# Performance work log

Hardware: AMD Instinct MI355X
Metric: run time of the kernel (lower is better)

## Reference

```python
import jax, jax.numpy as jnp
import numpy as np
import jax.scipy.signal as jss

SX, SY, C, K = 256, 256, 3, 10
C0 = [0, 0, 0, 1, 1, 1, 2, 2, 2, 0]
C1 = [[0, 1, 2, 9], [3, 4, 5], [6, 7, 8]]
DD, DT, SIGMA = 5, 0.2, 0.65

_KX = jnp.array([[-1., 0., 1.], [-2., 0., 2.], [-1., 0., 1.]])
_KY = _KX.T


def _conv2(A, Kf):
    # zero-padded 'same' 2D true convolution, vmapped over channel axis
    return jax.vmap(lambda a: jss.convolve2d(a, Kf, mode='same'), in_axes=2, out_axes=2)(A)


def sobel(A):
    # (X, Y, c) -> (X, Y, 2, c): [sobel_y, sobel_x] stacked on axis 2 (FlowLenia convention)
    return jnp.concatenate([_conv2(A, _KY)[:, :, None, :], _conv2(A, _KX)[:, :, None, :]], axis=2)


def growth(U, m, s):
    # bell(U,m,s)*2 - 1
    return jnp.exp(-((U - m) / s) ** 2 / 2.) * 2. - 1.


def get_kernels_fft(R, r, a, w, b):
    # FlowLenia kernel construction: ring distance -> smooth cutoff * sum-of-bumps, normalized, fft2(fftshift)
    mid = SX // 2
    xs = jnp.arange(-mid, mid, dtype=jnp.float32)
    D = jnp.sqrt(xs[:, None] ** 2 + xs[None, :] ** 2)            # (X, Y)
    Dk = D[..., None] / ((R + 15.) * r)                          # (X, Y, k)
    ker = (b * jnp.exp(-(Dk[..., None] - a) ** 2 / w)).sum(-1)   # (X, Y, k)
    sig = 0.5 * (jnp.tanh(-(Dk - 1.) * 10. / 2.) + 1.)           # sigmoid(-(D-1)*10)
    Kk = sig * ker
    nK = Kk / Kk.sum(axis=(0, 1), keepdims=True)
    return jnp.fft.fft2(jnp.fft.fftshift(nK, axes=(0, 1)), axes=(0, 1))


def _rt_apply(A, F):
    # Reintegration tracking with 'wall' border: flow-driven mass redistribution over a (2dd+1)^2 neighborhood
    ii = jnp.arange(SX, dtype=jnp.float32)
    pos = jnp.stack(jnp.meshgrid(ii, ii, indexing='ij'), axis=-1) + 0.5   # (X, Y, 2) cell centers
    ma = DD - SIGMA                                   # max flow magnitude
    mu = pos[..., None] + jnp.clip(DT * F, -ma, ma)   # (X, Y, 2, C) target centers
    mu = jnp.clip(mu, SIGMA, SX - SIGMA)              # wall border
    offs = jnp.arange(-DD, DD + 1)
    gx, gy = jnp.meshgrid(offs, offs, indexing='ij')
    dxs, dys = gx.reshape(-1), gy.reshape(-1)
    clip_hi = min(1., 2. * SIGMA)

    def step(dx, dy):
        Ar = jnp.roll(A, (dx, dy), axis=(0, 1))
        mur = jnp.roll(mu, (dx, dy), axis=(0, 1))
        dpmu = jnp.abs(pos[..., None] - mur)                                  # (X, Y, 2, C)
        sz = 0.5 - dpmu + SIGMA
        area = jnp.prod(jnp.clip(sz, 0., clip_hi), axis=2) / (4. * SIGMA ** 2)  # (X, Y, C)
        return Ar * area

    return jax.vmap(step)(dxs, dys).sum(axis=0)


def setup_inputs() -> dict:
    key = jax.random.key(0)
    ks = jax.random.split(key, 9)
    A = jax.random.uniform(ks[0], (SX, SY, C), dtype=jnp.float32)
    R = jax.random.uniform(ks[1], (), minval=2.0, maxval=25.0)
    r = jax.random.uniform(ks[2], (K,), minval=0.2, maxval=1.0)
    m = jax.random.uniform(ks[3], (K,), minval=0.05, maxval=0.5)
    s = jax.random.uniform(ks[4], (K,), minval=0.001, maxval=0.18)
    h = jax.random.uniform(ks[5], (K,), minval=0.01, maxval=1.0)
    a = jax.random.uniform(ks[6], (K, 3), minval=0.0, maxval=1.0)
    b = jax.random.uniform(ks[7], (K, 3), minval=0.001, maxval=1.0)
    w = jax.random.uniform(ks[8], (K, 3), minval=0.01, maxval=0.5)
    return dict(A=A, R=R, r=r, m=m, s=s, h=h, a=a, b=b, w=w)


def reference(A, R, r, m, s, h, a, b, w):
    fK = get_kernels_fft(R, r, a, w, b)                       # (X, Y, k) complex
    fA = jnp.fft.fft2(A, axes=(0, 1))
    fAk = fA[:, :, jnp.array(C0)]                             # (X, Y, k)
    U = jnp.real(jnp.fft.ifft2(fK * fAk, axes=(0, 1)))        # (X, Y, k)
    U = growth(U, m, s) * h
    U = jnp.dstack([U[:, :, C1[c]].sum(axis=-1) for c in range(C)])  # (X, Y, C)
    nabla_U = sobel(U)                                        # (X, Y, 2, C)
    nabla_A = sobel(A.sum(axis=-1, keepdims=True))            # (X, Y, 2, 1)
    alpha = jnp.clip((A[:, :, None, :] / C) ** 2, 0., 1.)     # (X, Y, 1, C)
    F = nabla_U * (1. - alpha) - nabla_A * alpha              # (X, Y, 2, C)
    return _rt_apply(A, F)
```

## Files before the change

kernel.cpp:

```cpp
#include <hip/hip_runtime.h>

#define NPIX 65536

#define WS_APLANE 0
#define WS_ASUM   (3*NPIX)
#define WS_KOFF   (4*NPIX)
#define WS_MUX    (4*NPIX)
#define WS_MUY    (7*NPIX)
#define WS_UACC   (14*NPIX)
#define WS_ROWS   (24*NPIX)
#define WS_X1RE   (25*NPIX)
#define WS_X1IM   (38*NPIX)
#define WS_X2RE   (51*NPIX)
#define WS_X2IM   (64*NPIX)
#define WS_END    (77*NPIX)

__global__ void k_prep(const float* __restrict__ A,
                       const float* __restrict__ R_, const float* __restrict__ r_,
                       const float* __restrict__ a_, const float* __restrict__ b_,
                       const float* __restrict__ w_, float* __restrict__ ws) {
    int bid = blockIdx.x;
    int t = threadIdx.x;
    if (bid < 256) {
        int idx = bid * 256 + t;
        float a0 = A[idx*3+0], a1 = A[idx*3+1], a2 = A[idx*3+2];
        ws[WS_APLANE + idx]          = a0;
        ws[WS_APLANE + NPIX + idx]   = a1;
        ws[WS_APLANE + 2*NPIX + idx] = a2;
        ws[WS_ASUM + idx] = a0 + a1 + a2;
        return;
    }
    __shared__ float red[256];
    int bk = bid - 256;
    int k = bk >> 8;
    int i = bk & 255;
    float R = R_[0];
    float denom = (R + 15.0f) * r_[k];
    int di = i - 128, dj = t - 128;
    float D  = sqrtf((float)(di*di + dj*dj));
    float Dk = D / denom;
    float ker = 0.0f;
    #pragma unroll
    for (int tt = 0; tt < 3; ++tt) {
        float d = Dk - a_[k*3+tt];
        ker += b_[k*3+tt] * expf(-((d*d) / w_[k*3+tt]));
    }
    float sig = 1.0f / (1.0f + expf(10.0f * (Dk - 1.0f)));
    float v = sig * ker;
    int iw = (i + 128) & 255;
    int jw = (t + 128) & 255;
    ws[WS_KOFF + k*NPIX + iw*256 + jw] = v;
    red[t] = v;
    __syncthreads();
    #pragma unroll
    for (int s = 128; s > 0; s >>= 1) {
        if (t < s) red[t] += red[t + s];
        __syncthreads();
    }
    if (t == 0) ws[WS_ROWS + k*256 + i] = red[0];
}

__device__ __forceinline__ void fft256_core(float* __restrict__ re, float* __restrict__ im,
                                            const float* __restrict__ twr,
                                            const float* __restrict__ twi, int lane) {
    #pragma unroll
    for (int s = 1; s <= 8; ++s) {
        int h = 1 << (s - 1);
        #pragma unroll
        for (int b = 0; b < 2; ++b) {
            int idx = b*64 + lane;
            int pos = idx & (h - 1);
            int g   = idx >> (s - 1);
            int i0 = (g << s) + pos;
            int i1 = i0 + h;
            int tj = pos << (8 - s);
            float wr = twr[tj], wi = twi[tj];
            float xr = re[i1], xi = im[i1];
            float br = fmaf(xr, wr, -xi*wi);
            float bi = fmaf(xr, wi,  xi*wr);
            float ar = re[i0], ai = im[i0];
            re[i0] = ar + br; im[i0] = ai + bi;
            re[i1] = ar - br; im[i1] = ai - bi;
        }
    }
}

__device__ __forceinline__ void build_tw(float* twr, float* twi, int t, float sgn) {
    if (t < 128) {
        float ang = (float)t * 0.0245436930f;
        twr[t] = cosf(ang);
        twi[t] = sgn * sinf(ang);
    }
}

__device__ __forceinline__ void store_t4(float* __restrict__ dst, const float* __restrict__ buf,
                                         int off, int t, int lb) {
    float4 v;
    v.x = buf[0*512 + off + t];
    v.y = buf[1*512 + off + t];
    v.z = buf[2*512 + off + t];
    v.w = buf[3*512 + off + t];
    *(float4*)&dst[t*256 + lb] = v;
}

__global__ __launch_bounds__(256) void fft_fwd_real(float* __restrict__ ws) {
    __shared__ float buf[4*512];
    __shared__ float twr[128], twi[128];
    int p  = blockIdx.x >> 6;
    int lb = (blockIdx.x & 63) * 4;
    int wid = threadIdx.x >> 6, lane = threadIdx.x & 63;
    int t = threadIdx.x;
    build_tw(twr, twi, t, -1.0f);
    const float* src = ws + ((p < 3) ? (WS_APLANE + p*NPIX) : (WS_KOFF + (p-3)*NPIX));
    float* re = &buf[wid*512];
    float* im = re + 256;
    const float* row = src + (lb + wid)*256;
    #pragma unroll
    for (int e = 0; e < 4; ++e) {
        int idx = e*64 + lane;
        int dst = __brev(idx) >> 24;
        re[dst] = row[idx];
        im[dst] = 0.0f;
    }
    __syncthreads();
    fft256_core(re, im, twr, twi, lane);
    __syncthreads();
    store_t4(ws + WS_X1RE + p*NPIX, buf, 0,   t, lb);
    store_t4(ws + WS_X1IM + p*NPIX, buf, 256, t, lb);
}

__global__ __launch_bounds__(256) void fft_fwd_cplx(float* __restrict__ ws) {
    __shared__ float buf[4*512];
    __shared__ float twr[128], twi[128];
    int p  = blockIdx.x >> 6;
    int lb = (blockIdx.x & 63) * 4;
    int wid = threadIdx.x >> 6, lane = threadIdx.x & 63;
    int t = threadIdx.x;
    build_tw(twr, twi, t, -1.0f);
    float* re = &buf[wid*512];
    float* im = re + 256;
    const float* rr = ws + WS_X1RE + p*NPIX + (lb + wid)*256;
    const float* ri = ws + WS_X1IM + p*NPIX + (lb + wid)*256;
    #pragma unroll
    for (int e = 0; e < 4; ++e) {
        int idx = e*64 + lane;
        int dst = __brev(idx) >> 24;
        re[dst] = rr[idx];
        im[dst] = ri[idx];
    }
    __syncthreads();
    fft256_core(re, im, twr, twi, lane);
    __syncthreads();
    store_t4(ws + WS_X2RE + p*NPIX, buf, 0,   t, lb);
    store_t4(ws + WS_X2IM + p*NPIX, buf, 256, t, lb);
}

__constant__ int C0K[10] = {0,0,0,1,1,1,2,2,2,0};

__global__ __launch_bounds__(256) void ifft_mul(float* __restrict__ ws) {
    __shared__ float buf[4*512];
    __shared__ float twr[128], twi[128];
    int k  = blockIdx.x >> 6;
    int lb = (blockIdx.x & 63) * 4;
    int wid = threadIdx.x >> 6, lane = threadIdx.x & 63;
    int t = threadIdx.x;
    build_tw(twr, twi, t, 1.0f);
    int c = (k < 9) ? (k / 3) : 0;
    int rowoff = (lb + wid)*256;
    const float* arp = ws + WS_X2RE + c*NPIX + rowoff;
    const float* aip = ws + WS_X2IM + c*NPIX + rowoff;
    const float* krp = ws + WS_X2RE + (3+k)*NPIX + rowoff;
    const float* kip = ws + WS_X2IM + (3+k)*NPIX + rowoff;
    float* re = &buf[wid*512];
    float* im = re + 256;
    #pragma unroll
    for (int e = 0; e < 4; ++e) {
        int idx = e*64 + lane;
        int dst = __brev(idx) >> 24;
        float ar = arp[idx], ai = aip[idx];
        float kr = krp[idx], ki = kip[idx];
        re[dst] = ar*kr - ai*ki;
        im[dst] = ar*ki + ai*kr;
    }
    __syncthreads();
    fft256_core(re, im, twr, twi, lane);
    __syncthreads();
    store_t4(ws + WS_X1RE + k*NPIX, buf, 0,   t, lb);
    store_t4(ws + WS_X1IM + k*NPIX, buf, 256, t, lb);
}

__global__ __launch_bounds__(256) void ifft_real(float* __restrict__ ws) {
    __shared__ float buf[4*512];
    __shared__ float twr[128], twi[128];
    int k  = blockIdx.x >> 6;
    int lb = (blockIdx.x & 63) * 4;
    int wid = threadIdx.x >> 6, lane = threadIdx.x & 63;
    int t = threadIdx.x;
    build_tw(twr, twi, t, 1.0f);
    float* re = &buf[wid*512];
    float* im = re + 256;
    const float* rr = ws + WS_X1RE + k*NPIX + (lb + wid)*256;
    const float* ri = ws + WS_X1IM + k*NPIX + (lb + wid)*256;
    #pragma unroll
    for (int e = 0; e < 4; ++e) {
        int idx = e*64 + lane;
        int dst = __brev(idx) >> 24;
        re[dst] = rr[idx];
        im[dst] = ri[idx];
    }
    __syncthreads();
    fft256_core(re, im, twr, twi, lane);
    __syncthreads();
    const float sc = 1.0f / 65536.0f;
    float4 v;
    v.x = buf[0*512 + t] * sc;
    v.y = buf[1*512 + t] * sc;
    v.z = buf[2*512 + t] * sc;
    v.w = buf[3*512 + t] * sc;
    *(float4*)&ws[WS_UACC + k*NPIX + t*256 + lb] = v;
}

__device__ inline void sobel_at(const float* __restrict__ p, int x, int y,
                                float& gy, float& gx) {
    float v[3][3];
    #pragma unroll
    for (int ii = -1; ii <= 1; ++ii)
        #pragma unroll
        for (int jj = -1; jj <= 1; ++jj) {
            int xx = x + ii, yy = y + jj;
            v[ii+1][jj+1] = (xx < 0 || xx > 255 || yy < 0 || yy > 255)
                            ? 0.0f : p[xx*256 + yy];
        }
    gy = (v[0][0] + 2.0f*v[0][1] + v[0][2]) - (v[2][0] + 2.0f*v[2][1] + v[2][2]);
    gx = (v[0][0] + 2.0f*v[1][0] + v[2][0]) - (v[0][2] + 2.0f*v[1][2] + v[2][2]);
}

__global__ __launch_bounds__(256) void growth_mu(float* __restrict__ ws,
                                                 const float* __restrict__ m_,
                                                 const float* __restrict__ s_,
                                                 const float* __restrict__ h_) {
    __shared__ float Ush[3][256];
    __shared__ float kinv[4];
    int b = blockIdx.x;
    int c = b >> 8;
    int x = b & 255;
    int t = threadIdx.x, wid = t >> 6, lane = t & 63;
    int nk = (c == 0) ? 4 : 3;
    if (wid < nk) {
        int k = (wid == 3) ? 9 : c*3 + wid;
        const float* rw = ws + WS_ROWS + k*256;
        float v = rw[lane] + rw[64+lane] + rw[128+lane] + rw[192+lane];
        #pragma unroll
        for (int off = 32; off; off >>= 1) v += __shfl_xor(v, off);
        if (lane == 0) kinv[wid] = 1.0f / v;
    }
    __syncthreads();
    const float* uacc = ws + WS_UACC;
    for (int rr = 0; rr < 3; ++rr) {
        int xr = x - 1 + rr;
        float outv = 0.0f;
        if (xr >= 0 && xr <= 255) {
            int idx = xr*256 + t;
            for (int kk = 0; kk < nk; ++kk) {
                int k = (kk == 3) ? 9 : c*3 + kk;
                float U = uacc[k*NPIX + idx] * kinv[kk];
                float z = (U - m_[k]) / s_[k];
                outv += h_[k] * (expf(-0.5f*z*z)*2.0f - 1.0f);
            }
        }
        Ush[rr][t] = outv;
    }
    __syncthreads();
    int y = t;
    float gyA, gxA;
    sobel_at(ws + WS_ASUM, x, y, gyA, gxA);
    float v[3][3];
    #pragma unroll
    for (int ii = -1; ii <= 1; ++ii)
        #pragma unroll
        for (int jj = -1; jj <= 1; ++jj) {
            int xx = x + ii, yy = y + jj;
            v[ii+1][jj+1] = (xx < 0 || xx > 255 || yy < 0 || yy > 255)
                            ? 0.0f : Ush[ii+1][yy];
        }
    float gy = (v[0][0] + 2.0f*v[0][1] + v[0][2]) - (v[2][0] + 2.0f*v[2][1] + v[2][2]);
    float gx = (v[0][0] + 2.0f*v[1][0] + v[2][0]) - (v[0][2] + 2.0f*v[1][2] + v[2][2]);
    float a = ws[WS_APLANE + c*NPIX + x*256 + y];
    float al = (a / 3.0f); al = al * al;
    al = fminf(fmaxf(al, 0.0f), 1.0f);
    float F0 = gy * (1.0f - al) - gyA * al;
    float F1 = gx * (1.0f - al) - gxA * al;
    float d0 = fminf(fmaxf(0.2f * F0, -4.35f), 4.35f);
    float d1 = fminf(fmaxf(0.2f * F1, -4.35f), 4.35f);
    ws[WS_MUX + c*NPIX + x*256 + y] = fminf(fmaxf((float)x + 0.5f + d0, 0.65f), 255.35f);
    ws[WS_MUY + c*NPIX + x*256 + y] = fminf(fmaxf((float)y + 0.5f + d1, 0.65f), 255.35f);
}

__global__ __launch_bounds__(256) void rt_apply_v2(const float* __restrict__ ws,
                                                   float* __restrict__ out) {
    __shared__ float sA[11*256], sX[11*256], sY[11*256];
    int b = blockIdx.x;
    int c = b >> 8;
    int x = b & 255;
    const float* ap = ws + WS_APLANE + c*NPIX;
    const float* mx = ws + WS_MUX + c*NPIX;
    const float* my = ws + WS_MUY + c*NPIX;
    int t = threadIdx.x;
    #pragma unroll
    for (int i = 0; i < 11; ++i) {
        int src = (((x - (i - 5)) & 255) << 8) + t;
        sA[i*256 + t] = ap[src];
        sX[i*256 + t] = mx[src];
        sY[i*256 + t] = my[src];
    }
    __syncthreads();
    int y = t;
    float px = (float)x + 0.5f, py = (float)y + 0.5f;
    float acc = 0.0f;
    #pragma unroll
    for (int dx = -5; dx <= 5; ++dx) {
        int rb = (dx + 5) * 256;
        for (int dy = -5; dy <= 5; ++dy) {
            int sy = (y - dy) & 255;
            float a  = sA[rb + sy];
            float ax = 1.15f - fabsf(px - sX[rb + sy]);
            float ay = 1.15f - fabsf(py - sY[rb + sy]);
            ax = fminf(fmaxf(ax, 0.0f), 1.0f);
            ay = fminf(fmaxf(ay, 0.0f), 1.0f);
            acc = fmaf(a, ax * ay, acc);
        }
    }
    out[(x*256 + y)*3 + c] = acc * (1.0f / (4.0f * 0.65f * 0.65f));
}

extern "C" void kernel_launch(void* const* d_in, const int* in_sizes, int n_in,
                              void* d_out, int out_size, void* d_ws, size_t ws_size,
                              hipStream_t stream) {
    const float* A = (const float*)d_in[0];
    const float* R = (const float*)d_in[1];
    const float* r = (const float*)d_in[2];
    const float* m = (const float*)d_in[3];
    const float* s = (const float*)d_in[4];
    const float* h = (const float*)d_in[5];
    const float* a = (const float*)d_in[6];
    const float* b = (const float*)d_in[7];
    const float* w = (const float*)d_in[8];
    float* ws  = (float*)d_ws;
    float* out = (float*)d_out;

    k_prep<<<256 + 2560, 256, 0, stream>>>(A, R, r, a, b, w, ws);
    fft_fwd_real<<<13*64, 256, 0, stream>>>(ws);
    fft_fwd_cplx<<<13*64, 256, 0, stream>>>(ws);
    ifft_mul<<<10*64, 256, 0, stream>>>(ws);
    ifft_real<<<10*64, 256, 0, stream>>>(ws);
    growth_mu<<<768, 256, 0, stream>>>(ws, m, s, h);
    rt_apply_v2<<<768, 256, 0, stream>>>(ws, out);
}
```

Baseline: 125.3 us.

## Pack pairs of real FFTs into single complex transforms

The forward row FFT now packs two real planes into the real and imaginary parts of one complex transform and separates them with conjugate-symmetry formulas, halving that launch's block count. The inverse pass packs pairs of spectral products as U_a + i*U_b, so the two inverse kernels run half as many blocks and the real outputs come out of the real and imaginary parts. Separately, kernel construction skips the exp evaluations when Dk > 3 and replaces the shared-memory tree reduction with wavefront shuffles. The Dk cutoff sets tiny but nonzero kernel values to zero, and the packing adds extra loads and arithmetic per block.

```diff
diff --git a/kernel.cpp b/kernel.cpp
--- a/kernel.cpp
+++ b/kernel.cpp
@@ -30,34 +30,36 @@
         ws[WS_ASUM + idx] = a0 + a1 + a2;
         return;
     }
-    __shared__ float red[256];
+    __shared__ float red[4];
     int bk = bid - 256;
     int k = bk >> 8;
     int i = bk & 255;
+    int wid = t >> 6, lane = t & 63;
     float R = R_[0];
     float denom = (R + 15.0f) * r_[k];
     int di = i - 128, dj = t - 128;
     float D  = sqrtf((float)(di*di + dj*dj));
     float Dk = D / denom;
-    float ker = 0.0f;
-    #pragma unroll
-    for (int tt = 0; tt < 3; ++tt) {
-        float d = Dk - a_[k*3+tt];
-        ker += b_[k*3+tt] * expf(-((d*d) / w_[k*3+tt]));
-    }
-    float sig = 1.0f / (1.0f + expf(10.0f * (Dk - 1.0f)));
-    float v = sig * ker;
+    float v = 0.0f;
+    if (Dk <= 3.0f) {
+        float ker = 0.0f;
+        #pragma unroll
+        for (int tt = 0; tt < 3; ++tt) {
+            float d = Dk - a_[k*3+tt];
+            ker += b_[k*3+tt] * expf(-((d*d) / w_[k*3+tt]));
+        }
+        float sig = 1.0f / (1.0f + expf(10.0f * (Dk - 1.0f)));
+        v = sig * ker;
+    }
     int iw = (i + 128) & 255;
     int jw = (t + 128) & 255;
     ws[WS_KOFF + k*NPIX + iw*256 + jw] = v;
-    red[t] = v;
-    __syncthreads();
-    #pragma unroll
-    for (int s = 128; s > 0; s >>= 1) {
-        if (t < s) red[t] += red[t + s];
-        __syncthreads();
-    }
-    if (t == 0) ws[WS_ROWS + k*256 + i] = red[0];
+    float s = v;
+    #pragma unroll
+    for (int off = 32; off; off >>= 1) s += __shfl_xor(s, off);
+    if (lane == 0) red[wid] = s;
+    __syncthreads();
+    if (t == 0) ws[WS_ROWS + k*256 + i] = red[0] + red[1] + red[2] + red[3];
 }
 
 __device__ __forceinline__ void fft256_core(float* __restrict__ re, float* __restrict__ im,
@@ -103,7 +105,7 @@
     *(float4*)&dst[t*256 + lb] = v;
 }
 
-__global__ __launch_bounds__(256) void fft_fwd_real(float* __restrict__ ws) {
+__global__ __launch_bounds__(256) void fft_fwd_packed(float* __restrict__ ws) {
     __shared__ float buf[4*512];
     __shared__ float twr[128], twi[128];
     int p  = blockIdx.x >> 6;
@@ -111,22 +113,42 @@
     int wid = threadIdx.x >> 6, lane = threadIdx.x & 63;
     int t = threadIdx.x;
     build_tw(twr, twi, t, -1.0f);
-    const float* src = ws + ((p < 3) ? (WS_APLANE + p*NPIX) : (WS_KOFF + (p-3)*NPIX));
+    int f = 2*p, g = 2*p + 1;
+    const float* frow = ws + ((f < 3) ? (WS_APLANE + f*NPIX) : (WS_KOFF + (f-3)*NPIX))
+                      + (lb + wid)*256;
+    const float* grow = (g < 13)
+        ? ws + ((g < 3) ? (WS_APLANE + g*NPIX) : (WS_KOFF + (g-3)*NPIX)) + (lb + wid)*256
+        : nullptr;
     float* re = &buf[wid*512];
     float* im = re + 256;
-    const float* row = src + (lb + wid)*256;
     #pragma unroll
     for (int e = 0; e < 4; ++e) {
         int idx = e*64 + lane;
         int dst = __brev(idx) >> 24;
-        re[dst] = row[idx];
-        im[dst] = 0.0f;
+        re[dst] = frow[idx];
+        im[dst] = grow ? grow[idx] : 0.0f;
     }
     __syncthreads();
     fft256_core(re, im, twr, twi, lane);
     __syncthreads();
-    store_t4(ws + WS_X1RE + p*NPIX, buf, 0,   t, lb);
-    store_t4(ws + WS_X1IM + p*NPIX, buf, 256, t, lb);
+    int u2 = (256 - t) & 255;
+    float4 Fre, Fim, Gre, Gim;
+    float* pF[4] = {&Fre.x, &Fim.x, &Gre.x, &Gim.x};
+    #pragma unroll
+    for (int l = 0; l < 4; ++l) {
+        float zr1 = buf[l*512 + t],  zi1 = buf[l*512 + 256 + t];
+        float zr2 = buf[l*512 + u2], zi2 = buf[l*512 + 256 + u2];
+        pF[0][l] = 0.5f*(zr1 + zr2);
+        pF[1][l] = 0.5f*(zi1 - zi2);
+        pF[2][l] = 0.5f*(zi1 + zi2);
+        pF[3][l] = 0.5f*(zr2 - zr1);
+    }
+    *(float4*)&ws[WS_X1RE + f*NPIX + t*256 + lb] = Fre;
+    *(float4*)&ws[WS_X1IM + f*NPIX + t*256 + lb] = Fim;
+    if (g < 13) {
+        *(float4*)&ws[WS_X1RE + g*NPIX + t*256 + lb] = Gre;
+        *(float4*)&ws[WS_X1IM + g*NPIX + t*256 + lb] = Gim;
+    }
 }
 
 __global__ __launch_bounds__(256) void fft_fwd_cplx(float* __restrict__ ws) {
@@ -155,22 +177,26 @@
     store_t4(ws + WS_X2IM + p*NPIX, buf, 256, t, lb);
 }
 
-__constant__ int C0K[10] = {0,0,0,1,1,1,2,2,2,0};
-
-__global__ __launch_bounds__(256) void ifft_mul(float* __restrict__ ws) {
+__global__ __launch_bounds__(256) void ifft_mul_packed(float* __restrict__ ws) {
     __shared__ float buf[4*512];
     __shared__ float twr[128], twi[128];
-    int k  = blockIdx.x >> 6;
+    int j  = blockIdx.x >> 6;
     int lb = (blockIdx.x & 63) * 4;
     int wid = threadIdx.x >> 6, lane = threadIdx.x & 63;
     int t = threadIdx.x;
     build_tw(twr, twi, t, 1.0f);
-    int c = (k < 9) ? (k / 3) : 0;
+    const int C0[10] = {0,0,0,1,1,1,2,2,2,0};
+    int ka = 2*j, kb = 2*j + 1;
+    int ca = C0[ka], cb = C0[kb];
     int rowoff = (lb + wid)*256;
-    const float* arp = ws + WS_X2RE + c*NPIX + rowoff;
-    const float* aip = ws + WS_X2IM + c*NPIX + rowoff;
-    const float* krp = ws + WS_X2RE + (3+k)*NPIX + rowoff;
-    const float* kip = ws + WS_X2IM + (3+k)*NPIX + rowoff;
+    const float* arp = ws + WS_X2RE + ca*NPIX + rowoff;
+    const float* aip = ws + WS_X2IM + ca*NPIX + rowoff;
+    const float* krp = ws + WS_X2RE + (3+ka)*NPIX + rowoff;
+    const float* kip = ws + WS_X2IM + (3+ka)*NPIX + rowoff;
+    const float* brp = ws + WS_X2RE + cb*NPIX + rowoff;
+    const float* bip = ws + WS_X2IM + cb*NPIX + rowoff;
+    const float* lrp = ws + WS_X2RE + (3+kb)*NPIX + rowoff;
+    const float* lip = ws + WS_X2IM + (3+kb)*NPIX + rowoff;
     float* re = &buf[wid*512];
     float* im = re + 256;
     #pragma unroll
@@ -179,28 +205,34 @@
         int dst = __brev(idx) >> 24;
         float ar = arp[idx], ai = aip[idx];
         float kr = krp[idx], ki = kip[idx];
-        re[dst] = ar*kr - ai*ki;
-        im[dst] = ar*ki + ai*kr;
+        float uar = ar*kr - ai*ki;
+        float uai = ar*ki + ai*kr;
+        float br = brp[idx], bi = bip[idx];
+        float lr = lrp[idx], li = lip[idx];
+        float ubr = br*lr - bi*li;
+        float ubi = br*li + bi*lr;
+        re[dst] = uar - ubi;
+        im[dst] = uai + ubr;
     }
     __syncthreads();
     fft256_core(re, im, twr, twi, lane);
     __syncthreads();
-    store_t4(ws + WS_X1RE + k*NPIX, buf, 0,   t, lb);
-    store_t4(ws + WS_X1IM + k*NPIX, buf, 256, t, lb);
-}
-
-__global__ __launch_bounds__(256) void ifft_real(float* __restrict__ ws) {
+    store_t4(ws + WS_X1RE + j*NPIX, buf, 0,   t, lb);
+    store_t4(ws + WS_X1IM + j*NPIX, buf, 256, t, lb);
+}
+
+__global__ __launch_bounds__(256) void ifft_real_packed(float* __restrict__ ws) {
     __shared__ float buf[4*512];
     __shared__ float twr[128], twi[128];
-    int k  = blockIdx.x >> 6;
+    int j  = blockIdx.x >> 6;
     int lb = (blockIdx.x & 63) * 4;
     int wid = threadIdx.x >> 6, lane = threadIdx.x & 63;
     int t = threadIdx.x;
     build_tw(twr, twi, t, 1.0f);
     float* re = &buf[wid*512];
     float* im = re + 256;
-    const float* rr = ws + WS_X1RE + k*NPIX + (lb + wid)*256;
-    const float* ri = ws + WS_X1IM + k*NPIX + (lb + wid)*256;
+    const float* rr = ws + WS_X1RE + j*NPIX + (lb + wid)*256;
+    const float* ri = ws + WS_X1IM + j*NPIX + (lb + wid)*256;
     #pragma unroll
     for (int e = 0; e < 4; ++e) {
         int idx = e*64 + lane;
@@ -212,12 +244,13 @@
     fft256_core(re, im, twr, twi, lane);
     __syncthreads();
     const float sc = 1.0f / 65536.0f;
-    float4 v;
-    v.x = buf[0*512 + t] * sc;
-    v.y = buf[1*512 + t] * sc;
-    v.z = buf[2*512 + t] * sc;
-    v.w = buf[3*512 + t] * sc;
-    *(float4*)&ws[WS_UACC + k*NPIX + t*256 + lb] = v;
+    float4 va, vb;
+    va.x = buf[0*512 + t] * sc;       vb.x = buf[0*512 + 256 + t] * sc;
+    va.y = buf[1*512 + t] * sc;       vb.y = buf[1*512 + 256 + t] * sc;
+    va.z = buf[2*512 + t] * sc;       vb.z = buf[2*512 + 256 + t] * sc;
+    va.w = buf[3*512 + t] * sc;       vb.w = buf[3*512 + 256 + t] * sc;
+    *(float4*)&ws[WS_UACC + (2*j)*NPIX   + t*256 + lb] = va;
+    *(float4*)&ws[WS_UACC + (2*j+1)*NPIX + t*256 + lb] = vb;
 }
 
 __device__ inline void sobel_at(const float* __restrict__ p, int x, int y,
@@ -349,10 +382,10 @@
     float* out = (float*)d_out;
 
     k_prep<<<256 + 2560, 256, 0, stream>>>(A, R, r, a, b, w, ws);
-    fft_fwd_real<<<13*64, 256, 0, stream>>>(ws);
+    fft_fwd_packed<<<7*64, 256, 0, stream>>>(ws);
     fft_fwd_cplx<<<13*64, 256, 0, stream>>>(ws);
-    ifft_mul<<<10*64, 256, 0, stream>>>(ws);
-    ifft_real<<<10*64, 256, 0, stream>>>(ws);
+    ifft_mul_packed<<<5*64, 256, 0, stream>>>(ws);
+    ifft_real_packed<<<5*64, 256, 0, stream>>>(ws);
     growth_mu<<<768, 256, 0, stream>>>(ws, m, s, h);
     rt_apply_v2<<<768, 256, 0, stream>>>(ws, out);
 }
```

New measurement: 122.5 us. -2.2%, faster.
